# Kernel tuning notes

Measured on AMD Instinct MI355X. Metric: run time of the kernel, lower is better.

Reference implementation:

```python
import jax, jax.numpy as jnp
import numpy as np

B, T, D, H, K = 2, 384, 512, 8, 48
HD = D // H  # head_dim = 64
LN_EPS = 1e-5


def setup_inputs() -> dict:
    key = jax.random.key(0)
    ks = jax.random.split(key, 6)
    def lin_w(k, out_d, in_d):
        return jax.random.normal(k, (out_d, in_d), jnp.float32) / np.sqrt(in_d).astype(np.float32)
    return {
        "x": jax.random.normal(ks[0], (B, T, D), jnp.float32),
        "g_w": lin_w(ks[1], H, D), "g_b": jnp.zeros((H,), jnp.float32),
        "sp_w": lin_w(ks[2], D, HD), "sp_b": jnp.zeros((D,), jnp.float32),
        "gate_w": lin_w(ks[3], D, D), "gate_b": jnp.zeros((D,), jnp.float32),
        "U_w": lin_w(ks[4], D, D), "U_b": jnp.zeros((D,), jnp.float32),
        "ln_g": jnp.ones((D,), jnp.float32), "ln_b": jnp.zeros((D,), jnp.float32),
    }


def reference(x, g_w, g_b, sp_w, sp_b, gate_w, gate_b, U_w, U_b, ln_g, ln_b):
    b, t, d = x.shape
    # head-split superposition
    phi = x.reshape(b, t, H, HD)                               # (B,T,H,hd)
    alpha = jax.nn.softmax(x @ g_w.T + g_b, axis=-1)           # (B,T,H)
    x_super = jnp.einsum('bth,bthd->btd', alpha, phi)          # (B,T,hd)
    x_super = x_super @ sp_w.T + sp_b                          # (B,T,D)
    # gated pairwise entanglement: interaction[b,i,j,:] = gate[b,i]*gate[b,j]
    gate = jax.nn.sigmoid(x_super @ gate_w.T + gate_b)         # (B,T,D)
    interaction = gate[:, :, None, :] * gate[:, None, :, :]    # (B,T,T,D)
    # top-k by L2 norm over feature dim, gather along j axis
    scores = jnp.sqrt(jnp.sum(interaction * interaction, axis=-1))  # (B,T,T)
    _, idx = jax.lax.top_k(scores, K)                          # (B,T,K)
    gathered = jnp.take_along_axis(interaction, idx[..., None], axis=2)  # (B,T,K,D)
    entangled = gathered.sum(axis=2)                           # (B,T,D)
    x_out = x_super + entangled
    y = x_out @ U_w.T + U_b
    mu = jnp.mean(y, axis=-1, keepdims=True)
    var = jnp.mean((y - mu) ** 2, axis=-1, keepdims=True)
    return ln_g * (y - mu) * jax.lax.rsqrt(var + LN_EPS) + ln_b
```

## Files before the change

### kernel.cpp

```cpp
#include <hip/hip_runtime.h>
#include <math.h>
#include <float.h>

#define B_ 2
#define T_ 384
#define D_ 512
#define H_ 8
#define HD_ 64
#define K_ 48
#define LN_EPS 1e-5f
#define NTOK (B_ * T_)
#define PART_STRIDE (NTOK * D_)

__global__ __launch_bounds__(256) void k_super(const float* __restrict__ x,
                                               const float* __restrict__ g_w,
                                               const float* __restrict__ g_b,
                                               const float* __restrict__ sp_w,
                                               const float* __restrict__ sp_b,
                                               float* __restrict__ xs) {
    int t0 = blockIdx.x * 4;
    int tid = threadIdx.x;
    __shared__ float xsh[4][D_];
    __shared__ float logits[4][H_];
    __shared__ float hd[4][HD_];
    ((float4*)&xsh[0][0])[tid] = ((const float4*)(x + (size_t)t0 * D_))[tid];
    ((float4*)&xsh[0][0])[tid + 256] = ((const float4*)(x + (size_t)t0 * D_))[tid + 256];
    __syncthreads();
    int tt = tid >> 6, hh = (tid >> 3) & 7, l8 = tid & 7;
    float p = 0.f;
#pragma unroll
    for (int i = 0; i < 64; ++i) {
        int k = l8 + i * 8;
        p += xsh[tt][k] * g_w[hh * D_ + k];
    }
    p += __shfl_xor(p, 1);
    p += __shfl_xor(p, 2);
    p += __shfl_xor(p, 4);
    if (l8 == 0) logits[tt][hh] = p + g_b[hh];
    __syncthreads();
    {
        int lane = tid & 63;
        float m = logits[tt][0];
#pragma unroll
        for (int h = 1; h < H_; ++h) m = fmaxf(m, logits[tt][h]);
        float e[H_];
        float sum = 0.f;
#pragma unroll
        for (int h = 0; h < H_; ++h) { e[h] = expf(logits[tt][h] - m); sum += e[h]; }
        float inv = 1.f / sum;
        float v = 0.f;
#pragma unroll
        for (int h = 0; h < H_; ++h) v += e[h] * inv * xsh[tt][h * HD_ + lane];
        hd[tt][lane] = v;
    }
    __syncthreads();
    {
        float2 bv = ((const float2*)sp_b)[tid];
        float2 acc[4] = {bv, bv, bv, bv};
        const float* w0 = sp_w + (size_t)(2 * tid) * HD_;
        const float* w1 = w0 + HD_;
#pragma unroll
        for (int k = 0; k < HD_; k += 2) {
            float2 a0 = *(const float2*)&w0[k];
            float2 a1 = *(const float2*)&w1[k];
#pragma unroll
            for (int t = 0; t < 4; ++t) {
                float h0 = hd[t][k], h1 = hd[t][k + 1];
                acc[t].x += h0 * a0.x + h1 * a0.y;
                acc[t].y += h0 * a1.x + h1 * a1.y;
            }
        }
#pragma unroll
        for (int t = 0; t < 4; ++t)
            ((float2*)xs)[(size_t)(t0 + t) * 256 + tid] = acc[t];
    }
}

__global__ __launch_bounds__(256) void k_wgemm_part(const float* __restrict__ in,
                                                    const float* __restrict__ W,
                                                    float* __restrict__ part) {
    int c0 = blockIdx.x * 64, r0 = blockIdx.y * 32;
    int kbase = blockIdx.z * 128;
    float* pout = part + (size_t)blockIdx.z * PART_STRIDE;
    int tid = threadIdx.x;
    int ry = tid >> 4, cx = tid & 15;
    __shared__ float A_shT[32][33];
    __shared__ float B_sh[32][65];
    float acc[2][4];
#pragma unroll
    for (int r = 0; r < 2; ++r)
#pragma unroll
        for (int c = 0; c < 4; ++c) acc[r][c] = 0.f;
    int asr = tid >> 3, asc = (tid & 7) * 4;
    int bsr = tid >> 2, bsk = (tid & 3) * 8;
    for (int k0 = kbase; k0 < kbase + 128; k0 += 32) {
        float4 a4 = *(const float4*)&in[(size_t)(r0 + asr) * D_ + k0 + asc];
        A_shT[asc + 0][asr] = a4.x;
        A_shT[asc + 1][asr] = a4.y;
        A_shT[asc + 2][asr] = a4.z;
        A_shT[asc + 3][asr] = a4.w;
        float4 b4a = *(const float4*)&W[(size_t)(c0 + bsr) * D_ + k0 + bsk];
        float4 b4b = *(const float4*)&W[(size_t)(c0 + bsr) * D_ + k0 + bsk + 4];
        B_sh[bsk + 0][bsr] = b4a.x;
        B_sh[bsk + 1][bsr] = b4a.y;
        B_sh[bsk + 2][bsr] = b4a.z;
        B_sh[bsk + 3][bsr] = b4a.w;
        B_sh[bsk + 4][bsr] = b4b.x;
        B_sh[bsk + 5][bsr] = b4b.y;
        B_sh[bsk + 6][bsr] = b4b.z;
        B_sh[bsk + 7][bsr] = b4b.w;
        __syncthreads();
#pragma unroll
        for (int kk = 0; kk < 32; ++kk) {
            float2 a2 = *(const float2*)&A_shT[kk][ry * 2];
            float4 b4 = *(const float4*)&B_sh[kk][cx * 4];
            acc[0][0] += a2.x * b4.x; acc[0][1] += a2.x * b4.y;
            acc[0][2] += a2.x * b4.z; acc[0][3] += a2.x * b4.w;
            acc[1][0] += a2.y * b4.x; acc[1][1] += a2.y * b4.y;
            acc[1][2] += a2.y * b4.z; acc[1][3] += a2.y * b4.w;
        }
        __syncthreads();
    }
#pragma unroll
    for (int r = 0; r < 2; ++r) {
        float4 o;
        o.x = acc[r][0];
        o.y = acc[r][1];
        o.z = acc[r][2];
        o.w = acc[r][3];
        *(float4*)&pout[(size_t)(r0 + ry * 2 + r) * D_ + c0 + cx * 4] = o;
    }
}

template <int MODE>
__global__ __launch_bounds__(256) void k_wred(const float* __restrict__ part,
                                              const float* __restrict__ bias,
                                              float* __restrict__ out) {
    int idx = blockIdx.x * 256 + threadIdx.x;
    const float4* p = (const float4*)part;
    float4 a = p[idx];
    float4 b = p[idx + PART_STRIDE / 4];
    float4 c = p[idx + 2 * (PART_STRIDE / 4)];
    float4 d = p[idx + 3 * (PART_STRIDE / 4)];
    float4 bb = ((const float4*)bias)[idx & 127];
    float4 s;
    s.x = a.x + b.x + c.x + d.x + bb.x;
    s.y = a.y + b.y + c.y + d.y + bb.y;
    s.z = a.z + b.z + c.z + d.z + bb.z;
    s.w = a.w + b.w + c.w + d.w + bb.w;
    if (MODE == 0) {
        s.x = 1.f / (1.f + expf(-s.x));
        s.y = 1.f / (1.f + expf(-s.y));
        s.z = 1.f / (1.f + expf(-s.z));
        s.w = 1.f / (1.f + expf(-s.w));
    }
    ((float4*)out)[idx] = s;
}

__global__ __launch_bounds__(256) void k_scores(const float* __restrict__ gate,
                                                float* __restrict__ scores) {
    int b = blockIdx.z;
    int i0 = blockIdx.y * 64, j0 = blockIdx.x * 64;
    int tid = threadIdx.x;
    int tx = tid & 15, ty = tid >> 4;
    __shared__ float Ash[16][68];
    __shared__ float Bsh[16][68];
    float acc[4][4];
#pragma unroll
    for (int r = 0; r < 4; ++r)
#pragma unroll
        for (int c = 0; c < 4; ++c) acc[r][c] = 0.f;
    const float* gb = gate + (size_t)b * T_ * D_;
    int sr = tid >> 2, sc4 = (tid & 3) * 4;
    for (int k0 = 0; k0 < D_; k0 += 16) {
        float4 av = *(const float4*)&gb[(size_t)(i0 + sr) * D_ + k0 + sc4];
        float4 bvv = *(const float4*)&gb[(size_t)(j0 + sr) * D_ + k0 + sc4];
        Ash[sc4 + 0][sr] = av.x * av.x;
        Ash[sc4 + 1][sr] = av.y * av.y;
        Ash[sc4 + 2][sr] = av.z * av.z;
        Ash[sc4 + 3][sr] = av.w * av.w;
        Bsh[sc4 + 0][sr] = bvv.x * bvv.x;
        Bsh[sc4 + 1][sr] = bvv.y * bvv.y;
        Bsh[sc4 + 2][sr] = bvv.z * bvv.z;
        Bsh[sc4 + 3][sr] = bvv.w * bvv.w;
        __syncthreads();
#pragma unroll
        for (int kk = 0; kk < 16; ++kk) {
            float4 a4 = *(const float4*)&Ash[kk][4 * ty];
            float4 b4 = *(const float4*)&Bsh[kk][4 * tx];
            float ar[4] = {a4.x, a4.y, a4.z, a4.w};
            float bc[4] = {b4.x, b4.y, b4.z, b4.w};
#pragma unroll
            for (int r = 0; r < 4; ++r)
#pragma unroll
                for (int c = 0; c < 4; ++c) acc[r][c] += ar[r] * bc[c];
        }
        __syncthreads();
    }
#pragma unroll
    for (int r = 0; r < 4; ++r) {
        float4 o;
        o.x = sqrtf(acc[r][0]);
        o.y = sqrtf(acc[r][1]);
        o.z = sqrtf(acc[r][2]);
        o.w = sqrtf(acc[r][3]);
        *(float4*)&scores[((size_t)b * T_ + (i0 + 4 * ty + r)) * T_ + j0 + 4 * tx] = o;
    }
}

__global__ __launch_bounds__(256) void k_topk(const float* __restrict__ scores,
                                              int* __restrict__ sel) {
    int tid = threadIdx.x;
    int wave = tid >> 6, lane = tid & 63;
    int row = blockIdx.x * 4 + wave;
    int b = row / T_;
    const float* srow = scores + (size_t)row * T_;
    float v[6];
#pragma unroll
    for (int q = 0; q < 6; ++q) v[q] = srow[q * 64 + lane];
    int keep = 0;
    for (int it = 0; it < K_; ++it) {
        float bv = v[0];
        int bq = 0;
#pragma unroll
        for (int q = 1; q < 6; ++q)
            if (v[q] > bv) { bv = v[q]; bq = q; }
        int bidx = bq * 64 + lane;
#pragma unroll
        for (int off = 1; off < 64; off <<= 1) {
            float ov = __shfl_xor(bv, off);
            int oi = __shfl_xor(bidx, off);
            if (ov > bv || (ov == bv && oi < bidx)) { bv = ov; bidx = oi; }
        }
        if (lane == (bidx & 63)) v[bidx >> 6] = -FLT_MAX;
        if (lane == it) keep = bidx;
    }
    if (lane < K_) sel[row * K_ + lane] = b * T_ + keep;
}

__global__ __launch_bounds__(256) void k_ent(const int* __restrict__ sel,
                                             const float* __restrict__ gate,
                                             const float* __restrict__ xs,
                                             float* __restrict__ xo) {
    int row = blockIdx.x;
    int tid = threadIdx.x;
    __shared__ int ssel[K_];
    if (tid < K_) ssel[tid] = sel[row * K_ + tid];
    __syncthreads();
    const float2* g2 = (const float2*)gate;
    float2 s = {0.f, 0.f};
#pragma unroll 8
    for (int n = 0; n < K_; ++n) {
        float2 g = g2[(size_t)ssel[n] * 256 + tid];
        s.x += g.x;
        s.y += g.y;
    }
    float2 gi = g2[(size_t)row * 256 + tid];
    float2 xv = ((const float2*)xs)[(size_t)row * 256 + tid];
    float2 o;
    o.x = xv.x + gi.x * s.x;
    o.y = xv.y + gi.y * s.y;
    ((float2*)xo)[(size_t)row * 256 + tid] = o;
}

__global__ __launch_bounds__(256) void k_ln(const float* __restrict__ y,
                                            const float* __restrict__ ln_g,
                                            const float* __restrict__ ln_b,
                                            float* __restrict__ out) {
    int t0 = blockIdx.x * 4;
    int tid = threadIdx.x;
    int wave = tid >> 6, lane = tid & 63;
    __shared__ float2 red4[4];
    float2 lg = ((const float2*)ln_g)[tid];
    float2 lb = ((const float2*)ln_b)[tid];
#pragma unroll
    for (int j = 0; j < 4; ++j) {
        float2 a = ((const float2*)y)[(size_t)(t0 + j) * 256 + tid];
        float2 sv;
        sv.x = a.x + a.y;
        sv.y = a.x * a.x + a.y * a.y;
#pragma unroll
        for (int off = 32; off > 0; off >>= 1) {
            sv.x += __shfl_xor(sv.x, off);
            sv.y += __shfl_xor(sv.y, off);
        }
        if (lane == 0) red4[wave] = sv;
        __syncthreads();
        float m1 = red4[0].x + red4[1].x + red4[2].x + red4[3].x;
        float m2 = red4[0].y + red4[1].y + red4[2].y + red4[3].y;
        __syncthreads();
        float mu = m1 * (1.f / D_);
        float var = fmaxf(m2 * (1.f / D_) - mu * mu, 0.f);
        float inv = rsqrtf(var + LN_EPS);
        float2 o;
        o.x = lg.x * (a.x - mu) * inv + lb.x;
        o.y = lg.y * (a.y - mu) * inv + lb.y;
        ((float2*)out)[(size_t)(t0 + j) * 256 + tid] = o;
    }
}

extern "C" void kernel_launch(void* const* d_in, const int* in_sizes, int n_in,
                              void* d_out, int out_size, void* d_ws, size_t ws_size,
                              hipStream_t stream) {
    const float* x      = (const float*)d_in[0];
    const float* g_w    = (const float*)d_in[1];
    const float* g_b    = (const float*)d_in[2];
    const float* sp_w   = (const float*)d_in[3];
    const float* sp_b   = (const float*)d_in[4];
    const float* gate_w = (const float*)d_in[5];
    const float* gate_b = (const float*)d_in[6];
    const float* U_w    = (const float*)d_in[7];
    const float* U_b    = (const float*)d_in[8];
    const float* ln_g   = (const float*)d_in[9];
    const float* ln_b   = (const float*)d_in[10];

    float* ws     = (float*)d_ws;
    float* xs     = ws;
    float* gate   = xs + 393216;
    float* scores = gate + 393216;
    float* xo     = scores + 294912;
    float* yb     = xo + 393216;
    int*   sel    = (int*)(yb + 393216);
    float* part   = (float*)(sel + 36864);

    k_super<<<NTOK / 4, 256, 0, stream>>>(x, g_w, g_b, sp_w, sp_b, xs);
    k_wgemm_part<<<dim3(D_ / 64, NTOK / 32, 4), 256, 0, stream>>>(xs, gate_w, part);
    k_wred<0><<<NTOK * D_ / 1024, 256, 0, stream>>>(part, gate_b, gate);
    k_scores<<<dim3(T_ / 64, T_ / 64, B_), 256, 0, stream>>>(gate, scores);
    k_topk<<<NTOK / 4, 256, 0, stream>>>(scores, sel);
    k_ent<<<NTOK, 256, 0, stream>>>(sel, gate, xs, xo);
    k_wgemm_part<<<dim3(D_ / 64, NTOK / 32, 4), 256, 0, stream>>>(xo, U_w, part);
    k_wred<1><<<NTOK * D_ / 1024, 256, 0, stream>>>(part, U_b, yb);
    k_ln<<<NTOK / 4, 256, 0, stream>>>(yb, ln_g, ln_b, (float*)d_out);
}
```

Measured before the change: 195.3 us.

## Split-K scores, fuse topk with entanglement and reduction with layernorm

Several changes at once. k_super now handles one token per block instead of four. Both weight GEMMs use 8-way split-K instead of 4-way. The score GEMM is split-K across 8 slices, with the reduction and sqrt moved into a new fused top-k plus entanglement kernel that runs one wave per row. The second partial-sum reduction is fused with layernorm, which drops two launches and the intermediate scores, sel and y buffers. The goal is more parallelism for the small GEMMs and fewer launches, at the cost of much larger partial-buffer traffic (8x partials) and reduction reads.

```diff
diff --git a/kernel.cpp b/kernel.cpp
--- a/kernel.cpp
+++ b/kernel.cpp
@@ -11,6 +11,7 @@
 #define LN_EPS 1e-5f
 #define NTOK (B_ * T_)
 #define PART_STRIDE (NTOK * D_)
+#define T2 (T_ * T_)
 
 __global__ __launch_bounds__(256) void k_super(const float* __restrict__ x,
                                                const float* __restrict__ g_w,
@@ -18,69 +19,60 @@
                                                const float* __restrict__ sp_w,
                                                const float* __restrict__ sp_b,
                                                float* __restrict__ xs) {
-    int t0 = blockIdx.x * 4;
+    int token = blockIdx.x;
     int tid = threadIdx.x;
-    __shared__ float xsh[4][D_];
-    __shared__ float logits[4][H_];
-    __shared__ float hd[4][HD_];
-    ((float4*)&xsh[0][0])[tid] = ((const float4*)(x + (size_t)t0 * D_))[tid];
-    ((float4*)&xsh[0][0])[tid + 256] = ((const float4*)(x + (size_t)t0 * D_))[tid + 256];
+    __shared__ float xsh[D_];
+    __shared__ float logits[H_];
+    __shared__ float hd[HD_];
+    const float* xt = x + (size_t)token * D_;
+    ((float2*)xsh)[tid] = ((const float2*)xt)[tid];
     __syncthreads();
-    int tt = tid >> 6, hh = (tid >> 3) & 7, l8 = tid & 7;
+    int h = tid >> 5, l = tid & 31;
     float p = 0.f;
 #pragma unroll
-    for (int i = 0; i < 64; ++i) {
-        int k = l8 + i * 8;
-        p += xsh[tt][k] * g_w[hh * D_ + k];
-    }
-    p += __shfl_xor(p, 1);
-    p += __shfl_xor(p, 2);
-    p += __shfl_xor(p, 4);
-    if (l8 == 0) logits[tt][hh] = p + g_b[hh];
+    for (int i = 0; i < 16; ++i) {
+        int k = l + 32 * i;
+        p += xsh[k] * g_w[h * D_ + k];
+    }
+#pragma unroll
+    for (int off = 16; off > 0; off >>= 1) p += __shfl_xor(p, off);
+    if (l == 0) logits[h] = p + g_b[h];
     __syncthreads();
-    {
-        int lane = tid & 63;
-        float m = logits[tt][0];
-#pragma unroll
-        for (int h = 1; h < H_; ++h) m = fmaxf(m, logits[tt][h]);
+    if (tid < HD_) {
+        float m = logits[0];
+#pragma unroll
+        for (int hh = 1; hh < H_; ++hh) m = fmaxf(m, logits[hh]);
         float e[H_];
         float sum = 0.f;
 #pragma unroll
-        for (int h = 0; h < H_; ++h) { e[h] = expf(logits[tt][h] - m); sum += e[h]; }
+        for (int hh = 0; hh < H_; ++hh) { e[hh] = expf(logits[hh] - m); sum += e[hh]; }
         float inv = 1.f / sum;
         float v = 0.f;
 #pragma unroll
-        for (int h = 0; h < H_; ++h) v += e[h] * inv * xsh[tt][h * HD_ + lane];
-        hd[tt][lane] = v;
+        for (int hh = 0; hh < H_; ++hh) v += e[hh] * inv * xsh[hh * HD_ + tid];
+        hd[tid] = v;
     }
     __syncthreads();
-    {
-        float2 bv = ((const float2*)sp_b)[tid];
-        float2 acc[4] = {bv, bv, bv, bv};
-        const float* w0 = sp_w + (size_t)(2 * tid) * HD_;
-        const float* w1 = w0 + HD_;
-#pragma unroll
-        for (int k = 0; k < HD_; k += 2) {
-            float2 a0 = *(const float2*)&w0[k];
-            float2 a1 = *(const float2*)&w1[k];
-#pragma unroll
-            for (int t = 0; t < 4; ++t) {
-                float h0 = hd[t][k], h1 = hd[t][k + 1];
-                acc[t].x += h0 * a0.x + h1 * a0.y;
-                acc[t].y += h0 * a1.x + h1 * a1.y;
-            }
-        }
-#pragma unroll
-        for (int t = 0; t < 4; ++t)
-            ((float2*)xs)[(size_t)(t0 + t) * 256 + tid] = acc[t];
-    }
+    float a0 = sp_b[tid], a1 = sp_b[tid + 256];
+    const float* w0 = sp_w + (size_t)tid * HD_;
+    const float* w1 = sp_w + (size_t)(tid + 256) * HD_;
+#pragma unroll
+    for (int k = 0; k < HD_; k += 4) {
+        float4 h4 = *(const float4*)&hd[k];
+        float4 u0 = *(const float4*)&w0[k];
+        float4 u1 = *(const float4*)&w1[k];
+        a0 += h4.x * u0.x + h4.y * u0.y + h4.z * u0.z + h4.w * u0.w;
+        a1 += h4.x * u1.x + h4.y * u1.y + h4.z * u1.z + h4.w * u1.w;
+    }
+    xs[(size_t)token * D_ + tid] = a0;
+    xs[(size_t)token * D_ + 256 + tid] = a1;
 }
 
 __global__ __launch_bounds__(256) void k_wgemm_part(const float* __restrict__ in,
                                                     const float* __restrict__ W,
                                                     float* __restrict__ part) {
     int c0 = blockIdx.x * 64, r0 = blockIdx.y * 32;
-    int kbase = blockIdx.z * 128;
+    int kbase = blockIdx.z * 64;
     float* pout = part + (size_t)blockIdx.z * PART_STRIDE;
     int tid = threadIdx.x;
     int ry = tid >> 4, cx = tid & 15;
@@ -93,7 +85,7 @@
         for (int c = 0; c < 4; ++c) acc[r][c] = 0.f;
     int asr = tid >> 3, asc = (tid & 7) * 4;
     int bsr = tid >> 2, bsk = (tid & 3) * 8;
-    for (int k0 = kbase; k0 < kbase + 128; k0 += 32) {
+    for (int k0 = kbase; k0 < kbase + 64; k0 += 32) {
         float4 a4 = *(const float4*)&in[(size_t)(r0 + asr) * D_ + k0 + asc];
         A_shT[asc + 0][asr] = a4.x;
         A_shT[asc + 1][asr] = a4.y;
@@ -132,34 +124,30 @@
     }
 }
 
-template <int MODE>
-__global__ __launch_bounds__(256) void k_wred(const float* __restrict__ part,
-                                              const float* __restrict__ bias,
-                                              float* __restrict__ out) {
+__global__ __launch_bounds__(256) void k_wred_sig(const float* __restrict__ part,
+                                                  const float* __restrict__ bias,
+                                                  float* __restrict__ out) {
     int idx = blockIdx.x * 256 + threadIdx.x;
     const float4* p = (const float4*)part;
-    float4 a = p[idx];
-    float4 b = p[idx + PART_STRIDE / 4];
-    float4 c = p[idx + 2 * (PART_STRIDE / 4)];
-    float4 d = p[idx + 3 * (PART_STRIDE / 4)];
+    float4 s = {0.f, 0.f, 0.f, 0.f};
+#pragma unroll
+    for (int q = 0; q < 8; ++q) {
+        float4 a = p[idx + q * (PART_STRIDE / 4)];
+        s.x += a.x; s.y += a.y; s.z += a.z; s.w += a.w;
+    }
     float4 bb = ((const float4*)bias)[idx & 127];
-    float4 s;
-    s.x = a.x + b.x + c.x + d.x + bb.x;
-    s.y = a.y + b.y + c.y + d.y + bb.y;
-    s.z = a.z + b.z + c.z + d.z + bb.z;
-    s.w = a.w + b.w + c.w + d.w + bb.w;
-    if (MODE == 0) {
-        s.x = 1.f / (1.f + expf(-s.x));
-        s.y = 1.f / (1.f + expf(-s.y));
-        s.z = 1.f / (1.f + expf(-s.z));
-        s.w = 1.f / (1.f + expf(-s.w));
-    }
+    s.x = 1.f / (1.f + expf(-(s.x + bb.x)));
+    s.y = 1.f / (1.f + expf(-(s.y + bb.y)));
+    s.z = 1.f / (1.f + expf(-(s.z + bb.z)));
+    s.w = 1.f / (1.f + expf(-(s.w + bb.w)));
     ((float4*)out)[idx] = s;
 }
 
-__global__ __launch_bounds__(256) void k_scores(const float* __restrict__ gate,
-                                                float* __restrict__ scores) {
-    int b = blockIdx.z;
+__global__ __launch_bounds__(256) void k_scores_part(const float* __restrict__ gate,
+                                                     float* __restrict__ spart) {
+    int z = blockIdx.z;
+    int b = z >> 3, ks = z & 7;
+    int kbase = ks * 64;
     int i0 = blockIdx.y * 64, j0 = blockIdx.x * 64;
     int tid = threadIdx.x;
     int tx = tid & 15, ty = tid >> 4;
@@ -172,7 +160,7 @@
         for (int c = 0; c < 4; ++c) acc[r][c] = 0.f;
     const float* gb = gate + (size_t)b * T_ * D_;
     int sr = tid >> 2, sc4 = (tid & 3) * 4;
-    for (int k0 = 0; k0 < D_; k0 += 16) {
+    for (int k0 = kbase; k0 < kbase + 64; k0 += 16) {
         float4 av = *(const float4*)&gb[(size_t)(i0 + sr) * D_ + k0 + sc4];
         float4 bvv = *(const float4*)&gb[(size_t)(j0 + sr) * D_ + k0 + sc4];
         Ash[sc4 + 0][sr] = av.x * av.x;
@@ -197,27 +185,35 @@
         }
         __syncthreads();
     }
+    float* sp = spart + (size_t)z * T2;
 #pragma unroll
     for (int r = 0; r < 4; ++r) {
         float4 o;
-        o.x = sqrtf(acc[r][0]);
-        o.y = sqrtf(acc[r][1]);
-        o.z = sqrtf(acc[r][2]);
-        o.w = sqrtf(acc[r][3]);
-        *(float4*)&scores[((size_t)b * T_ + (i0 + 4 * ty + r)) * T_ + j0 + 4 * tx] = o;
-    }
-}
-
-__global__ __launch_bounds__(256) void k_topk(const float* __restrict__ scores,
-                                              int* __restrict__ sel) {
-    int tid = threadIdx.x;
-    int wave = tid >> 6, lane = tid & 63;
-    int row = blockIdx.x * 4 + wave;
+        o.x = acc[r][0];
+        o.y = acc[r][1];
+        o.z = acc[r][2];
+        o.w = acc[r][3];
+        *(float4*)&sp[(size_t)(i0 + 4 * ty + r) * T_ + j0 + 4 * tx] = o;
+    }
+}
+
+__global__ __launch_bounds__(64) void k_topk_ent(const float* __restrict__ spart,
+                                                 const float* __restrict__ gate,
+                                                 const float* __restrict__ xs,
+                                                 float* __restrict__ xo) {
+    int row = blockIdx.x;
     int b = row / T_;
-    const float* srow = scores + (size_t)row * T_;
+    int i = row - b * T_;
+    int lane = threadIdx.x;
     float v[6];
 #pragma unroll
-    for (int q = 0; q < 6; ++q) v[q] = srow[q * 64 + lane];
+    for (int q = 0; q < 6; ++q) {
+        float s = 0.f;
+#pragma unroll
+        for (int ks = 0; ks < 8; ++ks)
+            s += spart[(size_t)(b * 8 + ks) * T2 + (size_t)i * T_ + q * 64 + lane];
+        v[q] = sqrtf(s);
+    }
     int keep = 0;
     for (int it = 0; it < K_; ++it) {
         float bv = v[0];
@@ -235,68 +231,68 @@
         if (lane == (bidx & 63)) v[bidx >> 6] = -FLT_MAX;
         if (lane == it) keep = bidx;
     }
-    if (lane < K_) sel[row * K_ + lane] = b * T_ + keep;
-}
-
-__global__ __launch_bounds__(256) void k_ent(const int* __restrict__ sel,
-                                             const float* __restrict__ gate,
-                                             const float* __restrict__ xs,
-                                             float* __restrict__ xo) {
-    int row = blockIdx.x;
+    float4 s0 = {0.f, 0.f, 0.f, 0.f}, s1 = {0.f, 0.f, 0.f, 0.f};
+    const float* gb = gate + (size_t)b * T_ * D_;
+    for (int n = 0; n < K_; ++n) {
+        int j = __shfl(keep, n);
+        const float4* gj = (const float4*)(gb + (size_t)j * D_ + lane * 8);
+        float4 g0 = gj[0], g1 = gj[1];
+        s0.x += g0.x; s0.y += g0.y; s0.z += g0.z; s0.w += g0.w;
+        s1.x += g1.x; s1.y += g1.y; s1.z += g1.z; s1.w += g1.w;
+    }
+    size_t base = (size_t)row * D_ + lane * 8;
+    const float4* gi = (const float4*)(gate + base);
+    const float4* xi = (const float4*)(xs + base);
+    float4 gi0 = gi[0], gi1 = gi[1];
+    float4 x0 = xi[0], x1 = xi[1];
+    x0.x += gi0.x * s0.x; x0.y += gi0.y * s0.y; x0.z += gi0.z * s0.z; x0.w += gi0.w * s0.w;
+    x1.x += gi1.x * s1.x; x1.y += gi1.y * s1.y; x1.z += gi1.z * s1.z; x1.w += gi1.w * s1.w;
+    float4* xov = (float4*)(xo + base);
+    xov[0] = x0;
+    xov[1] = x1;
+}
+
+__global__ __launch_bounds__(256) void k_wred_ln(const float* __restrict__ part,
+                                                 const float* __restrict__ U_b,
+                                                 const float* __restrict__ ln_g,
+                                                 const float* __restrict__ ln_b,
+                                                 float* __restrict__ out) {
     int tid = threadIdx.x;
-    __shared__ int ssel[K_];
-    if (tid < K_) ssel[tid] = sel[row * K_ + tid];
+    int idx = blockIdx.x * 256 + tid;
+    const float4* p = (const float4*)part;
+    float4 s = {0.f, 0.f, 0.f, 0.f};
+#pragma unroll
+    for (int q = 0; q < 8; ++q) {
+        float4 a = p[idx + q * (PART_STRIDE / 4)];
+        s.x += a.x; s.y += a.y; s.z += a.z; s.w += a.w;
+    }
+    float4 ub = ((const float4*)U_b)[tid & 127];
+    s.x += ub.x; s.y += ub.y; s.z += ub.z; s.w += ub.w;
+    float sum = s.x + s.y + s.z + s.w;
+    float sq = s.x * s.x + s.y * s.y + s.z * s.z + s.w * s.w;
+#pragma unroll
+    for (int off = 32; off > 0; off >>= 1) {
+        sum += __shfl_xor(sum, off);
+        sq += __shfl_xor(sq, off);
+    }
+    __shared__ float red[4][2];
+    int wave = tid >> 6;
+    if ((tid & 63) == 0) { red[wave][0] = sum; red[wave][1] = sq; }
     __syncthreads();
-    const float2* g2 = (const float2*)gate;
-    float2 s = {0.f, 0.f};
-#pragma unroll 8
-    for (int n = 0; n < K_; ++n) {
-        float2 g = g2[(size_t)ssel[n] * 256 + tid];
-        s.x += g.x;
-        s.y += g.y;
-    }
-    float2 gi = g2[(size_t)row * 256 + tid];
-    float2 xv = ((const float2*)xs)[(size_t)row * 256 + tid];
-    float2 o;
-    o.x = xv.x + gi.x * s.x;
-    o.y = xv.y + gi.y * s.y;
-    ((float2*)xo)[(size_t)row * 256 + tid] = o;
-}
-
-__global__ __launch_bounds__(256) void k_ln(const float* __restrict__ y,
-                                            const float* __restrict__ ln_g,
-                                            const float* __restrict__ ln_b,
-                                            float* __restrict__ out) {
-    int t0 = blockIdx.x * 4;
-    int tid = threadIdx.x;
-    int wave = tid >> 6, lane = tid & 63;
-    __shared__ float2 red4[4];
-    float2 lg = ((const float2*)ln_g)[tid];
-    float2 lb = ((const float2*)ln_b)[tid];
-#pragma unroll
-    for (int j = 0; j < 4; ++j) {
-        float2 a = ((const float2*)y)[(size_t)(t0 + j) * 256 + tid];
-        float2 sv;
-        sv.x = a.x + a.y;
-        sv.y = a.x * a.x + a.y * a.y;
-#pragma unroll
-        for (int off = 32; off > 0; off >>= 1) {
-            sv.x += __shfl_xor(sv.x, off);
-            sv.y += __shfl_xor(sv.y, off);
-        }
-        if (lane == 0) red4[wave] = sv;
-        __syncthreads();
-        float m1 = red4[0].x + red4[1].x + red4[2].x + red4[3].x;
-        float m2 = red4[0].y + red4[1].y + red4[2].y + red4[3].y;
-        __syncthreads();
-        float mu = m1 * (1.f / D_);
-        float var = fmaxf(m2 * (1.f / D_) - mu * mu, 0.f);
-        float inv = rsqrtf(var + LN_EPS);
-        float2 o;
-        o.x = lg.x * (a.x - mu) * inv + lb.x;
-        o.y = lg.y * (a.y - mu) * inv + lb.y;
-        ((float2*)out)[(size_t)(t0 + j) * 256 + tid] = o;
-    }
+    int rw = (tid >> 7) * 2;
+    float m1 = red[rw][0] + red[rw + 1][0];
+    float m2 = red[rw][1] + red[rw + 1][1];
+    float mu = m1 * (1.f / D_);
+    float var = fmaxf(m2 * (1.f / D_) - mu * mu, 0.f);
+    float inv = rsqrtf(var + LN_EPS);
+    float4 lg = ((const float4*)ln_g)[tid & 127];
+    float4 lb = ((const float4*)ln_b)[tid & 127];
+    float4 o;
+    o.x = lg.x * (s.x - mu) * inv + lb.x;
+    o.y = lg.y * (s.y - mu) * inv + lb.y;
+    o.z = lg.z * (s.z - mu) * inv + lb.z;
+    o.w = lg.w * (s.w - mu) * inv + lb.w;
+    ((float4*)out)[idx] = o;
 }
 
 extern "C" void kernel_launch(void* const* d_in, const int* in_sizes, int n_in,
@@ -314,22 +310,18 @@
     const float* ln_g   = (const float*)d_in[9];
     const float* ln_b   = (const float*)d_in[10];
 
-    float* ws     = (float*)d_ws;
-    float* xs     = ws;
-    float* gate   = xs + 393216;
-    float* scores = gate + 393216;
-    float* xo     = scores + 294912;
-    float* yb     = xo + 393216;
-    int*   sel    = (int*)(yb + 393216);
-    float* part   = (float*)(sel + 36864);
-
-    k_super<<<NTOK / 4, 256, 0, stream>>>(x, g_w, g_b, sp_w, sp_b, xs);
-    k_wgemm_part<<<dim3(D_ / 64, NTOK / 32, 4), 256, 0, stream>>>(xs, gate_w, part);
-    k_wred<0><<<NTOK * D_ / 1024, 256, 0, stream>>>(part, gate_b, gate);
-    k_scores<<<dim3(T_ / 64, T_ / 64, B_), 256, 0, stream>>>(gate, scores);
-    k_topk<<<NTOK / 4, 256, 0, stream>>>(scores, sel);
-    k_ent<<<NTOK, 256, 0, stream>>>(sel, gate, xs, xo);
-    k_wgemm_part<<<dim3(D_ / 64, NTOK / 32, 4), 256, 0, stream>>>(xo, U_w, part);
-    k_wred<1><<<NTOK * D_ / 1024, 256, 0, stream>>>(part, U_b, yb);
-    k_ln<<<NTOK / 4, 256, 0, stream>>>(yb, ln_g, ln_b, (float*)d_out);
-}
+    float* ws    = (float*)d_ws;
+    float* xs    = ws;
+    float* gate  = xs + 393216;
+    float* xo    = gate + 393216;
+    float* part  = xo + 393216;
+    float* spart = part + 8 * 393216;
+
+    k_super<<<NTOK, 256, 0, stream>>>(x, g_w, g_b, sp_w, sp_b, xs);
+    k_wgemm_part<<<dim3(D_ / 64, NTOK / 32, 8), 256, 0, stream>>>(xs, gate_w, part);
+    k_wred_sig<<<NTOK * D_ / 1024, 256, 0, stream>>>(part, gate_b, gate);
+    k_scores_part<<<dim3(T_ / 64, T_ / 64, 16), 256, 0, stream>>>(gate, spart);
+    k_topk_ent<<<NTOK, 64, 0, stream>>>(spart, gate, xs, xo);
+    k_wgemm_part<<<dim3(D_ / 64, NTOK / 32, 8), 256, 0, stream>>>(xo, U_w, part);
+    k_wred_ln<<<NTOK * D_ / 1024, 256, 0, stream>>>(part, U_b, ln_g, ln_b, (float*)d_out);
+}
```

Result: faster. 181.0 us (-7.3%).
